# Optimization experiments

Measured on AMD Instinct MI355X. Metric: run time of the kernel, lower is better.

The kernel has to match this reference:

```python
import jax, jax.numpy as jnp
import numpy as np

N_NODES = 100000
N_EDGES = 1600000
N_FEAT = 128
HIDDEN = 128
N_GRAPHS = 100


def setup_inputs() -> dict:
    key = jax.random.key(0)
    ks = jax.random.split(key, 12)
    glorot = lambda k, fi, fo: jax.random.normal(k, (fo, fi), jnp.float32) * (1.0 / np.sqrt(fi))
    x = jax.random.normal(ks[0], (N_NODES, N_FEAT), jnp.float32)
    edge_index = jax.random.randint(ks[1], (2, N_EDGES), 0, N_NODES, jnp.int64)
    batch = jnp.sort(jax.random.randint(ks[2], (N_NODES,), 0, N_GRAPHS, jnp.int64))
    return {
        "x": x,
        "edge_index": edge_index,
        "batch": batch,
        "W1": glorot(ks[3], N_FEAT, HIDDEN), "b1": jnp.zeros((HIDDEN,), jnp.float32),
        "W2": glorot(ks[4], HIDDEN, HIDDEN), "b2": jnp.zeros((HIDDEN,), jnp.float32),
        "W3": glorot(ks[5], HIDDEN, HIDDEN), "b3": jnp.zeros((HIDDEN,), jnp.float32),
        "W4": glorot(ks[6], HIDDEN, HIDDEN), "b4": jnp.zeros((HIDDEN,), jnp.float32),
    }


def _aggregate(x, edge_index):
    # GIN aggregation with eps=0: (1+eps)*x_i + sum_{j in N(i)} x_j
    src, dst = edge_index[0], edge_index[1]
    agg = jax.ops.segment_sum(x[src], dst, num_segments=N_NODES)
    return x + agg


def _mlp(h, Wa, ba, Wb, bb):
    h = jax.nn.relu(h @ Wa.T + ba)
    return jax.nn.relu(h @ Wb.T + bb)


def reference(x, edge_index, batch, W1, b1, W2, b2, W3, b3, W4, b4):
    # conv1: GINConv(MLP1), then extra relu (no-op after MLP's relu), dropout in eval = identity
    h = _mlp(_aggregate(x, edge_index), W1, b1, W2, b2)
    # conv2: GINConv(MLP2), then relu
    h = _mlp(_aggregate(h, edge_index), W3, b3, W4, b4)
    # global mean pool over graphs
    sums = jax.ops.segment_sum(h, batch, num_segments=N_GRAPHS)
    counts = jax.ops.segment_sum(jnp.ones((h.shape[0],), h.dtype), batch, num_segments=N_GRAPHS)
    x_pool = sums / jnp.maximum(counts, 1.0)[:, None]
    return (x_pool, h)
```

## Files before the change

### kernel.cpp

```cpp
#include <hip/hip_runtime.h>

#define N_NODES  100000
#define N_EDGES  1600000
#define NF       128
#define N_GRAPHS 100
#define NBKT     391
#define BKT_SHIFT 8
#define CAP      6144
#define CAPN     48
#define EPB      4096
#define EB_GRID  391

typedef __attribute__((ext_vector_type(8))) short bf16x8;
typedef __attribute__((ext_vector_type(4))) float f32x4;
typedef __attribute__((ext_vector_type(2))) float f32x2;
typedef unsigned int uint32;

__device__ __forceinline__ unsigned short f2bf(float f) {
    union { float f; uint32 u; } x; x.f = f;
    return (unsigned short)((x.u + 0x7fffu + ((x.u >> 16) & 1u)) >> 16);
}
__device__ __forceinline__ uint32 pack2bf(float a, float b) {
    union { float f; uint32 u; } x, y; x.f = a; y.f = b;
    uint32 lo = (x.u + 0x7fffu + ((x.u >> 16) & 1u)) >> 16;
    uint32 hi = (y.u + 0x7fffu + ((y.u >> 16) & 1u)) & 0xffff0000u;
    return lo | hi;
}
__device__ __forceinline__ void add8(f32x2* acc, uint4 u4) {
    uint32 u[4] = {u4.x, u4.y, u4.z, u4.w};
    #pragma unroll
    for (int i = 0; i < 4; ++i) {
        union { uint32 b; float f; } lo, hi;
        lo.b = u[i] << 16; hi.b = u[i] & 0xffff0000u;
        acc[i] += (f32x2){lo.f, hi.f};
    }
}

__global__ __launch_bounds__(256) void prep(const float4* __restrict__ x,
                                            const float4* __restrict__ w1,
                                            const float4* __restrict__ w2,
                                            const float4* __restrict__ w3,
                                            const float4* __restrict__ w4,
                                            uint4* __restrict__ xb, uint4* __restrict__ wb,
                                            int* __restrict__ cur, float* __restrict__ sums) {
    int bid = blockIdx.x, t = threadIdx.x;
    if (bid < 6250) {
        int i = bid * 256 + t;
        float4 a = x[i * 2], b = x[i * 2 + 1];
        uint4 o;
        o.x = pack2bf(a.x, a.y); o.y = pack2bf(a.z, a.w);
        o.z = pack2bf(b.x, b.y); o.w = pack2bf(b.z, b.w);
        xb[i] = o;
    } else if (bid < 6282) {
        int i = (bid - 6250) * 256 + t;
        int wi = i >> 11, li = i & 2047;
        const float4* s = (wi == 0) ? w1 : (wi == 1) ? w2 : (wi == 2) ? w3 : w4;
        float4 a = s[li * 2], b = s[li * 2 + 1];
        uint4 o;
        o.x = pack2bf(a.x, a.y); o.y = pack2bf(a.z, a.w);
        o.z = pack2bf(b.x, b.y); o.w = pack2bf(b.z, b.w);
        wb[i] = o;
    } else {
        int idx = (bid - 6282) * 256 + t;
        for (int i = idx; i < N_GRAPHS * NF; i += 4096) sums[i] = 0.f;
        if (idx < NBKT) cur[idx] = 0;
    }
}

__global__ __launch_bounds__(512) void bscatter(const int* __restrict__ src,
                                                const int* __restrict__ dst,
                                                int* __restrict__ cur,
                                                uint32* __restrict__ ebuf) {
    __shared__ int lh[NBKT], lbase[NBKT];
    int t = threadIdx.x;
    if (t < NBKT) lh[t] = 0;
    __syncthreads();
    int e0 = blockIdx.x * EPB;
    int d[8];
    #pragma unroll
    for (int i = 0; i < 8; ++i) {
        int e = e0 + i * 512 + t;
        d[i] = -1;
        if (e < N_EDGES) { d[i] = dst[e]; atomicAdd(&lh[d[i] >> BKT_SHIFT], 1); }
    }
    __syncthreads();
    if (t < NBKT) { lbase[t] = t * CAP + atomicAdd(&cur[t], lh[t]); lh[t] = 0; }
    __syncthreads();
    #pragma unroll
    for (int i = 0; i < 8; ++i) {
        int e = e0 + i * 512 + t;
        if (e < N_EDGES) {
            int b = d[i] >> BKT_SHIFT;
            int off = atomicAdd(&lh[b], 1);
            ebuf[lbase[b] + off] = ((uint32)(d[i] & 255) << 17) | (uint32)src[e];
        }
    }
}

__global__ __launch_bounds__(256) void bfine(const uint32* __restrict__ ebuf,
                                             const int* __restrict__ cur,
                                             int* __restrict__ cnt,
                                             int* __restrict__ csr) {
    __shared__ int off[256];
    int t = threadIdx.x;
    int bkt = blockIdx.x;
    int beg = bkt * CAP;
    int end = beg + cur[bkt];
    off[t] = 0;
    __syncthreads();
    for (int e = beg + t; e < end; e += 256) {
        uint32 u = ebuf[e];
        int local = (int)(u >> 17);
        int pos = atomicAdd(&off[local], 1);
        if (pos < CAPN)
            csr[((bkt << BKT_SHIFT) + local) * CAPN + pos] = (int)(u & 0x1FFFFu);
    }
    __syncthreads();
    int node = (bkt << BKT_SHIFT) + t;
    if (node < N_NODES) cnt[node] = min(off[t], CAPN);
}

__global__ __launch_bounds__(256) void gather_agg_bf16(const uint4* __restrict__ x,
                                                       const int* __restrict__ cnt,
                                                       const int* __restrict__ csr,
                                                       uint4* __restrict__ out) {
    int gid  = blockIdx.x * 256 + threadIdx.x;
    int node = gid >> 6;
    int l = threadIdx.x & 63;
    int c = l & 15;
    int j = l >> 4;
    int beg = node * CAPN;

    uint4 vself = x[(size_t)node * 16 + c];
    int myE = csr[beg + min(l, CAPN - 1)];
    int deg = cnt[node];

    f32x2 acc[4];
    #pragma unroll
    for (int i = 0; i < 4; ++i) acc[i] = (f32x2){0.f, 0.f};

    uint4 v[8];
    int ok[8];
    #pragma unroll
    for (int k = 0; k < 4; ++k) {
        int sl = j + 4 * k;
        int sle = max(min(sl, deg - 1), 0);
        unsigned s = (unsigned)__shfl(myE, sle, 64);
        s = min(s, (unsigned)(N_NODES - 1));
        v[k] = x[(size_t)s * 16 + c];
        ok[k] = sl < deg;
    }
    if (deg > 16) {
        #pragma unroll
        for (int k = 0; k < 4; ++k) {
            int sl = 16 + j + 4 * k;
            int sle = min(sl, deg - 1);
            unsigned s = (unsigned)__shfl(myE, sle, 64);
            s = min(s, (unsigned)(N_NODES - 1));
            v[4 + k] = x[(size_t)s * 16 + c];
            ok[4 + k] = sl < deg;
        }
    }
    #pragma unroll
    for (int k = 0; k < 4; ++k) if (ok[k]) add8(acc, v[k]);
    if (deg > 16) {
        #pragma unroll
        for (int k = 0; k < 4; ++k) if (ok[4 + k]) add8(acc, v[4 + k]);
        for (int sl0 = 32; sl0 < deg; sl0 += 16) {
            #pragma unroll
            for (int k = 0; k < 4; ++k) {
                int sl = sl0 + j + 4 * k;
                int sle = min(sl, deg - 1);
                unsigned s = (unsigned)__shfl(myE, sle, 64);
                s = min(s, (unsigned)(N_NODES - 1));
                uint4 vv = x[(size_t)s * 16 + c];
                if (sl < deg) add8(acc, vv);
            }
        }
    }

    #pragma unroll
    for (int i = 0; i < 4; ++i) {
        acc[i].x += __shfl_xor(acc[i].x, 16, 64);
        acc[i].y += __shfl_xor(acc[i].y, 16, 64);
        acc[i].x += __shfl_xor(acc[i].x, 32, 64);
        acc[i].y += __shfl_xor(acc[i].y, 32, 64);
    }

    add8(acc, vself);

    if (j == 0) {
        uint4 o;
        o.x = pack2bf(acc[0].x, acc[0].y); o.y = pack2bf(acc[1].x, acc[1].y);
        o.z = pack2bf(acc[2].x, acc[2].y); o.w = pack2bf(acc[3].x, acc[3].y);
        out[(size_t)node * 16 + c] = o;
    }
}

template <bool F32OUT>
__global__ __launch_bounds__(256, 4) void mlp_mfma(const unsigned short* __restrict__ A,
                                                   const unsigned short* __restrict__ Wa,
                                                   const float* __restrict__ ba,
                                                   const unsigned short* __restrict__ Wb,
                                                   const float* __restrict__ bb,
                                                   void* __restrict__ Cout, int M) {
    __shared__ unsigned short Mid[128 * 136];
    int tid  = threadIdx.x;
    int row0 = blockIdx.x * 128;
    int wv = tid >> 6, l = tid & 63, lm = l & 15, q = l >> 4;

    const unsigned short* pa0 = A + (size_t)min(row0 + wv * 32 + lm,      M - 1) * NF;
    const unsigned short* pa1 = A + (size_t)min(row0 + wv * 32 + 16 + lm, M - 1) * NF;
    const unsigned short* pwa = Wa + lm * NF;
    const unsigned short* pwb = Wb + lm * NF;

    f32x4 acc[2][8];
    #pragma unroll
    for (int i = 0; i < 2; ++i)
        #pragma unroll
        for (int j = 0; j < 8; ++j) acc[i][j] = (f32x4){0.f, 0.f, 0.f, 0.f};

    #pragma unroll
    for (int ks = 0; ks < 4; ++ks) {
        int ko = ks * 32 + q * 8;
        bf16x8 a0 = *(const bf16x8*)(pa0 + ko);
        bf16x8 a1 = *(const bf16x8*)(pa1 + ko);
        #pragma unroll
        for (int ct = 0; ct < 8; ++ct) {
            bf16x8 b = *(const bf16x8*)(pwa + ct * 16 * NF + ko);
            acc[0][ct] = __builtin_amdgcn_mfma_f32_16x16x32_bf16(a0, b, acc[0][ct], 0, 0, 0);
            acc[1][ct] = __builtin_amdgcn_mfma_f32_16x16x32_bf16(a1, b, acc[1][ct], 0, 0, 0);
        }
    }

    #pragma unroll
    for (int rt = 0; rt < 2; ++rt)
        #pragma unroll
        for (int ct = 0; ct < 8; ++ct) {
            int col = ct * 16 + lm;
            float bv = ba[col];
            #pragma unroll
            for (int r = 0; r < 4; ++r) {
                int rr = wv * 32 + rt * 16 + q * 4 + r;
                Mid[rr * 136 + col] = f2bf(fmaxf(acc[rt][ct][r] + bv, 0.f));
            }
        }
    __syncthreads();

    #pragma unroll
    for (int i = 0; i < 2; ++i)
        #pragma unroll
        for (int j = 0; j < 8; ++j) acc[i][j] = (f32x4){0.f, 0.f, 0.f, 0.f};

    const unsigned short* pm0 = &Mid[(wv * 32 + lm) * 136];
    const unsigned short* pm1 = &Mid[(wv * 32 + 16 + lm) * 136];
    #pragma unroll
    for (int ks = 0; ks < 4; ++ks) {
        int ko = ks * 32 + q * 8;
        bf16x8 a0 = *(const bf16x8*)(pm0 + ko);
        bf16x8 a1 = *(const bf16x8*)(pm1 + ko);
        #pragma unroll
        for (int ct = 0; ct < 8; ++ct) {
            bf16x8 b = *(const bf16x8*)(pwb + ct * 16 * NF + ko);
            acc[0][ct] = __builtin_amdgcn_mfma_f32_16x16x32_bf16(a0, b, acc[0][ct], 0, 0, 0);
            acc[1][ct] = __builtin_amdgcn_mfma_f32_16x16x32_bf16(a1, b, acc[1][ct], 0, 0, 0);
        }
    }

    #pragma unroll
    for (int rt = 0; rt < 2; ++rt)
        #pragma unroll
        for (int ct = 0; ct < 8; ++ct) {
            int col = ct * 16 + lm;
            float bv = bb[col];
            #pragma unroll
            for (int r = 0; r < 4; ++r) {
                int row = row0 + wv * 32 + rt * 16 + q * 4 + r;
                if (row < M) {
                    float v = fmaxf(acc[rt][ct][r] + bv, 0.f);
                    if (F32OUT) ((float*)Cout)[(size_t)row * NF + col] = v;
                    else ((unsigned short*)Cout)[(size_t)row * NF + col] = f2bf(v);
                }
            }
        }
}

__global__ __launch_bounds__(256) void pool_sum2(const float* __restrict__ h,
                                                 const int* __restrict__ batch,
                                                 float* __restrict__ sums) {
    int t = threadIdx.x;
    int f = t & 127, seg = t >> 7;
    int n0 = blockIdx.x * 128 + seg * 64;
    if (n0 >= N_NODES) return;
    int n1 = min(n0 + 64, N_NODES);
    int cur = batch[n0];
    float acc = 0.f;
    for (int n = n0; n < n1; ++n) {
        int g = batch[n];
        if (g != cur) {
            atomicAdd(&sums[cur * NF + f], acc);
            acc = 0.f; cur = g;
        }
        acc += h[(size_t)n * NF + f];
    }
    atomicAdd(&sums[cur * NF + f], acc);
}

__global__ __launch_bounds__(256) void pool_div2(const float* __restrict__ sums,
                                                 const int* __restrict__ batch,
                                                 float* __restrict__ out) {
    int i = blockIdx.x * 256 + threadIdx.x;
    if (i >= N_GRAPHS * NF) return;
    int g = i >> 7;
    int lo = 0, hi = N_NODES;
    while (lo < hi) { int m = (lo + hi) >> 1; if (batch[m] < g) lo = m + 1; else hi = m; }
    int lo2 = lo, hi2 = N_NODES;
    while (lo2 < hi2) { int m = (lo2 + hi2) >> 1; if (batch[m] < g + 1) lo2 = m + 1; else hi2 = m; }
    float cnt = (float)(lo2 - lo);
    out[i] = sums[i] / fmaxf(cnt, 1.f);
}

extern "C" void kernel_launch(void* const* d_in, const int* in_sizes, int n_in,
                              void* d_out, int out_size, void* d_ws, size_t ws_size,
                              hipStream_t stream) {
    const float* x     = (const float*)d_in[0];
    const int*   ei    = (const int*)d_in[1];
    const int*   batch = (const int*)d_in[2];
    const float* W1 = (const float*)d_in[3];  const float* b1 = (const float*)d_in[4];
    const float* W2 = (const float*)d_in[5];  const float* b2 = (const float*)d_in[6];
    const float* W3 = (const float*)d_in[7];  const float* b3 = (const float*)d_in[8];
    const float* W4 = (const float*)d_in[9];  const float* b4 = (const float*)d_in[10];
    const int* src = ei;
    const int* dst = ei + N_EDGES;

    float* out   = (float*)d_out;
    float* h_out = out + N_GRAPHS * NF;

    const size_t NE = (size_t)N_NODES * NF;
    unsigned short* xb = (unsigned short*)d_ws;
    unsigned short* t0 = xb + NE;
    unsigned short* t1 = t0 + NE;
    unsigned short* Wb = t1 + NE;
    int*    csr  = (int*)(Wb + 4 * NF * NF);
    int*    cntp = csr + (size_t)N_NODES * CAPN;
    int*    curp = cntp + N_NODES;
    float*  sums = (float*)(curp + NBKT);
    uint32* ebuf = (uint32*)t1;

    const int gather_blocks = N_NODES * 64 / 256;
    const int gemm_blocks   = (N_NODES + 127) / 128;

    prep<<<6250 + 32 + 16, 256, 0, stream>>>((const float4*)x,
                                             (const float4*)W1, (const float4*)W2,
                                             (const float4*)W3, (const float4*)W4,
                                             (uint4*)xb, (uint4*)Wb, curp, sums);

    bscatter<<<EB_GRID, 512, 0, stream>>>(src, dst, curp, ebuf);
    bfine<<<NBKT, 256, 0, stream>>>(ebuf, curp, cntp, csr);

    gather_agg_bf16<<<gather_blocks, 256, 0, stream>>>((const uint4*)xb, cntp, csr, (uint4*)t0);
    mlp_mfma<false><<<gemm_blocks, 256, 0, stream>>>(t0, Wb + 0 * NF * NF, b1,
                                                     Wb + 1 * NF * NF, b2, t1, N_NODES);

    gather_agg_bf16<<<gather_blocks, 256, 0, stream>>>((const uint4*)t1, cntp, csr, (uint4*)t0);
    mlp_mfma<true ><<<gemm_blocks, 256, 0, stream>>>(t0, Wb + 2 * NF * NF, b3,
                                                     Wb + 3 * NF * NF, b4, h_out, N_NODES);

    pool_sum2<<<(N_NODES + 127) / 128, 256, 0, stream>>>(h_out, batch, sums);
    pool_div2<<<(N_GRAPHS * NF + 255) / 256, 256, 0, stream>>>(sums, batch, out);
}
```

Baseline: 394.7 us.

## Fuse x bf16 conversion into bucket scatter, split fine sort, vectorize pooling

The fp32-to-bf16 conversion of x moves from the prep kernel into bscatter, which now handles half as many edges per block over twice as many blocks and skips atomics for empty buckets. bfine splits each bucket across two blocks, builds the per-node CSR in shared memory and writes it out with coalesced 16-byte stores, and clamps the bucket count to CAP. Pooling now reads float4 rows over shorter node segments. Together these aim to cut launch work and scattered global writes, but the fused kernel has more global traffic per block, and full padded CSR tiles are now written even for unused slots.

```diff
diff --git a/kernel.cpp b/kernel.cpp
--- a/kernel.cpp
+++ b/kernel.cpp
@@ -8,8 +8,9 @@
 #define BKT_SHIFT 8
 #define CAP      6144
 #define CAPN     48
-#define EPB      4096
-#define EB_GRID  391
+#define EPB      2048
+#define EB_GRID  782
+#define XCONV    2048
 
 typedef __attribute__((ext_vector_type(8))) short bf16x8;
 typedef __attribute__((ext_vector_type(4))) float f32x4;
@@ -36,23 +37,15 @@
     }
 }
 
-__global__ __launch_bounds__(256) void prep(const float4* __restrict__ x,
-                                            const float4* __restrict__ w1,
+__global__ __launch_bounds__(256) void prep(const float4* __restrict__ w1,
                                             const float4* __restrict__ w2,
                                             const float4* __restrict__ w3,
                                             const float4* __restrict__ w4,
-                                            uint4* __restrict__ xb, uint4* __restrict__ wb,
+                                            uint4* __restrict__ wb,
                                             int* __restrict__ cur, float* __restrict__ sums) {
     int bid = blockIdx.x, t = threadIdx.x;
-    if (bid < 6250) {
+    if (bid < 32) {
         int i = bid * 256 + t;
-        float4 a = x[i * 2], b = x[i * 2 + 1];
-        uint4 o;
-        o.x = pack2bf(a.x, a.y); o.y = pack2bf(a.z, a.w);
-        o.z = pack2bf(b.x, b.y); o.w = pack2bf(b.z, b.w);
-        xb[i] = o;
-    } else if (bid < 6282) {
-        int i = (bid - 6250) * 256 + t;
         int wi = i >> 11, li = i & 2047;
         const float4* s = (wi == 0) ? w1 : (wi == 1) ? w2 : (wi == 2) ? w3 : w4;
         float4 a = s[li * 2], b = s[li * 2 + 1];
@@ -61,7 +54,7 @@
         o.z = pack2bf(b.x, b.y); o.w = pack2bf(b.z, b.w);
         wb[i] = o;
     } else {
-        int idx = (bid - 6282) * 256 + t;
+        int idx = (bid - 32) * 256 + t;
         for (int i = idx; i < N_GRAPHS * NF; i += 4096) sums[i] = 0.f;
         if (idx < NBKT) cur[idx] = 0;
     }
@@ -70,24 +63,39 @@
 __global__ __launch_bounds__(512) void bscatter(const int* __restrict__ src,
                                                 const int* __restrict__ dst,
                                                 int* __restrict__ cur,
-                                                uint32* __restrict__ ebuf) {
+                                                uint32* __restrict__ ebuf,
+                                                const float4* __restrict__ x,
+                                                uint4* __restrict__ xb) {
     __shared__ int lh[NBKT], lbase[NBKT];
     int t = threadIdx.x;
     if (t < NBKT) lh[t] = 0;
+
+    #pragma unroll
+    for (int k = 0; k < 4; ++k) {
+        int i = blockIdx.x * XCONV + k * 512 + t;
+        if (i < N_NODES * (NF / 8)) {
+            float4 a = x[i * 2], b = x[i * 2 + 1];
+            uint4 o;
+            o.x = pack2bf(a.x, a.y); o.y = pack2bf(a.z, a.w);
+            o.z = pack2bf(b.x, b.y); o.w = pack2bf(b.z, b.w);
+            xb[i] = o;
+        }
+    }
+
     __syncthreads();
     int e0 = blockIdx.x * EPB;
-    int d[8];
-    #pragma unroll
-    for (int i = 0; i < 8; ++i) {
+    int d[4];
+    #pragma unroll
+    for (int i = 0; i < 4; ++i) {
         int e = e0 + i * 512 + t;
         d[i] = -1;
         if (e < N_EDGES) { d[i] = dst[e]; atomicAdd(&lh[d[i] >> BKT_SHIFT], 1); }
     }
     __syncthreads();
-    if (t < NBKT) { lbase[t] = t * CAP + atomicAdd(&cur[t], lh[t]); lh[t] = 0; }
-    __syncthreads();
-    #pragma unroll
-    for (int i = 0; i < 8; ++i) {
+    if (t < NBKT) { lbase[t] = t * CAP + (lh[t] ? atomicAdd(&cur[t], lh[t]) : 0); lh[t] = 0; }
+    __syncthreads();
+    #pragma unroll
+    for (int i = 0; i < 4; ++i) {
         int e = e0 + i * 512 + t;
         if (e < N_EDGES) {
             int b = d[i] >> BKT_SHIFT;
@@ -101,23 +109,34 @@
                                              const int* __restrict__ cur,
                                              int* __restrict__ cnt,
                                              int* __restrict__ csr) {
-    __shared__ int off[256];
+    __shared__ int off[128];
+    __shared__ __align__(16) int lcsr[128 * CAPN];
     int t = threadIdx.x;
-    int bkt = blockIdx.x;
+    int bkt  = blockIdx.x >> 1;
+    int half = blockIdx.x & 1;
     int beg = bkt * CAP;
-    int end = beg + cur[bkt];
-    off[t] = 0;
+    int end = beg + min(cur[bkt], CAP);
+    if (t < 128) off[t] = 0;
     __syncthreads();
     for (int e = beg + t; e < end; e += 256) {
         uint32 u = ebuf[e];
         int local = (int)(u >> 17);
-        int pos = atomicAdd(&off[local], 1);
-        if (pos < CAPN)
-            csr[((bkt << BKT_SHIFT) + local) * CAPN + pos] = (int)(u & 0x1FFFFu);
-    }
-    __syncthreads();
-    int node = (bkt << BKT_SHIFT) + t;
-    if (node < N_NODES) cnt[node] = min(off[t], CAPN);
+        if ((local >> 7) == half) {
+            int li = local & 127;
+            int pos = atomicAdd(&off[li], 1);
+            if (pos < CAPN)
+                lcsr[li * CAPN + pos] = (int)(u & 0x1FFFFu);
+        }
+    }
+    __syncthreads();
+    if (t < 128) {
+        int node = (bkt << BKT_SHIFT) + (half << 7) + t;
+        if (node < N_NODES) cnt[node] = min(off[t], CAPN);
+    }
+    uint4* dstq = (uint4*)(csr + ((size_t)(bkt << BKT_SHIFT) + (half << 7)) * CAPN);
+    const uint4* srcq = (const uint4*)lcsr;
+    for (int i = t; i < 128 * CAPN / 4; i += 256)
+        dstq[i] = srcq[i];
 }
 
 __global__ __launch_bounds__(256) void gather_agg_bf16(const uint4* __restrict__ x,
@@ -285,25 +304,32 @@
         }
 }
 
-__global__ __launch_bounds__(256) void pool_sum2(const float* __restrict__ h,
+__global__ __launch_bounds__(256) void pool_sum4(const float4* __restrict__ h,
                                                  const int* __restrict__ batch,
                                                  float* __restrict__ sums) {
     int t = threadIdx.x;
-    int f = t & 127, seg = t >> 7;
-    int n0 = blockIdx.x * 128 + seg * 64;
+    int f4 = t & 31, seg = t >> 5;
+    int n0 = blockIdx.x * 128 + seg * 16;
     if (n0 >= N_NODES) return;
-    int n1 = min(n0 + 64, N_NODES);
+    int n1 = min(n0 + 16, N_NODES);
     int cur = batch[n0];
-    float acc = 0.f;
+    float4 acc = {0.f, 0.f, 0.f, 0.f};
     for (int n = n0; n < n1; ++n) {
         int g = batch[n];
         if (g != cur) {
-            atomicAdd(&sums[cur * NF + f], acc);
-            acc = 0.f; cur = g;
-        }
-        acc += h[(size_t)n * NF + f];
-    }
-    atomicAdd(&sums[cur * NF + f], acc);
+            atomicAdd(&sums[cur * NF + f4 * 4 + 0], acc.x);
+            atomicAdd(&sums[cur * NF + f4 * 4 + 1], acc.y);
+            atomicAdd(&sums[cur * NF + f4 * 4 + 2], acc.z);
+            atomicAdd(&sums[cur * NF + f4 * 4 + 3], acc.w);
+            acc = (float4){0.f, 0.f, 0.f, 0.f}; cur = g;
+        }
+        float4 v = h[(size_t)n * 32 + f4];
+        acc.x += v.x; acc.y += v.y; acc.z += v.z; acc.w += v.w;
+    }
+    atomicAdd(&sums[cur * NF + f4 * 4 + 0], acc.x);
+    atomicAdd(&sums[cur * NF + f4 * 4 + 1], acc.y);
+    atomicAdd(&sums[cur * NF + f4 * 4 + 2], acc.z);
+    atomicAdd(&sums[cur * NF + f4 * 4 + 3], acc.w);
 }
 
 __global__ __launch_bounds__(256) void pool_div2(const float* __restrict__ sums,
@@ -342,7 +368,7 @@
     unsigned short* t1 = t0 + NE;
     unsigned short* Wb = t1 + NE;
     int*    csr  = (int*)(Wb + 4 * NF * NF);
-    int*    cntp = csr + (size_t)N_NODES * CAPN;
+    int*    cntp = csr + (size_t)NBKT * 256 * CAPN;
     int*    curp = cntp + N_NODES;
     float*  sums = (float*)(curp + NBKT);
     uint32* ebuf = (uint32*)t1;
@@ -350,13 +376,12 @@
     const int gather_blocks = N_NODES * 64 / 256;
     const int gemm_blocks   = (N_NODES + 127) / 128;
 
-    prep<<<6250 + 32 + 16, 256, 0, stream>>>((const float4*)x,
-                                             (const float4*)W1, (const float4*)W2,
-                                             (const float4*)W3, (const float4*)W4,
-                                             (uint4*)xb, (uint4*)Wb, curp, sums);
-
-    bscatter<<<EB_GRID, 512, 0, stream>>>(src, dst, curp, ebuf);
-    bfine<<<NBKT, 256, 0, stream>>>(ebuf, curp, cntp, csr);
+    prep<<<32 + 16, 256, 0, stream>>>((const float4*)W1, (const float4*)W2,
+                                      (const float4*)W3, (const float4*)W4,
+                                      (uint4*)Wb, curp, sums);
+
+    bscatter<<<EB_GRID, 512, 0, stream>>>(src, dst, curp, ebuf, (const float4*)x, (uint4*)xb);
+    bfine<<<NBKT * 2, 256, 0, stream>>>(ebuf, curp, cntp, csr);
 
     gather_agg_bf16<<<gather_blocks, 256, 0, stream>>>((const uint4*)xb, cntp, csr, (uint4*)t0);
     mlp_mfma<false><<<gemm_blocks, 256, 0, stream>>>(t0, Wb + 0 * NF * NF, b1,
@@ -366,6 +391,6 @@
     mlp_mfma<true ><<<gemm_blocks, 256, 0, stream>>>(t0, Wb + 2 * NF * NF, b3,
                                                      Wb + 3 * NF * NF, b4, h_out, N_NODES);
 
-    pool_sum2<<<(N_NODES + 127) / 128, 256, 0, stream>>>(h_out, batch, sums);
+    pool_sum4<<<(N_NODES + 127) / 128, 256, 0, stream>>>((const float4*)h_out, batch, sums);
     pool_div2<<<(N_GRAPHS * NF + 255) / 256, 256, 0, stream>>>(sums, batch, out);
 }
```

Result: slower. 413.1 us (+4.7%).
